# Kernel tuning notes

Hardware: AMD Instinct MI355X
Metric: run time of the kernel (lower is better)

## Reference

```python
import jax, jax.numpy as jnp
import numpy as np

EPS = 1e-5


def setup_inputs() -> dict:
    key = jax.random.key(0)
    ks = jax.random.split(key, 4)
    N, E, D, L = 100000, 1600000, 128, 3
    x = jax.random.normal(ks[0], (N, D), dtype=jnp.float32)
    edge_index = jax.random.randint(ks[1], (2, E), 0, N, dtype=jnp.int64)
    # torch Linear weight layout [out, in]; kaiming-ish scale
    W = jax.random.normal(ks[2], (L, D, D), dtype=jnp.float32) / np.sqrt(D)
    b = jnp.zeros((L, D), dtype=jnp.float32)
    gamma = jnp.ones((L, D), dtype=jnp.float32)
    beta = jnp.zeros((L, D), dtype=jnp.float32)
    return {"x": x, "edge_index": edge_index, "W": W, "b": b,
            "gamma": gamma, "beta": beta}


def reference(x, edge_index, W, b, gamma, beta):
    N = x.shape[0]
    L = W.shape[0]
    # add_self_loops
    loops = jnp.arange(N, dtype=edge_index.dtype)
    ei = jnp.concatenate([edge_index, jnp.stack([loops, loops])], axis=1)
    row, col = ei[0], ei[1]  # source, target (PyG source_to_target flow)
    # degree of target nodes (includes self loops)
    deg = jax.ops.segment_sum(jnp.ones(col.shape, x.dtype), col, num_segments=N)
    deg_inv_sqrt = jnp.where(deg > 0, deg ** -0.5, jnp.array(0.0, x.dtype))
    norm = deg_inv_sqrt[row] * deg_inv_sqrt[col]  # [E+N]
    for l in range(L):
        h = x @ W[l].T  # Linear, no bias
        # gather source messages, scale, scatter-add to targets
        out = jax.ops.segment_sum(norm[:, None] * h[row], col, num_segments=N)
        out = out + b[l]
        # NodeNorm 'm': subtract per-node (row) mean over features
        out = out - jnp.mean(out, axis=1, keepdims=True)
        # BatchNorm1d (training mode: biased batch stats over node axis)
        mu = jnp.mean(out, axis=0)
        var = jnp.var(out, axis=0)
        x = gamma[l] * (out - mu) * jax.lax.rsqrt(var + EPS) + beta[l]
    return x
```

## Files before the change

### kernel.cpp

```cpp
#include <hip/hip_runtime.h>

#define D 128
#define EPSV 1e-5f

typedef _Float16 f16;
typedef __attribute__((ext_vector_type(8))) _Float16 f16x8;
typedef __attribute__((ext_vector_type(4))) _Float16 f16x4;
typedef __attribute__((ext_vector_type(4))) float f32x4;

__global__ __launch_bounds__(256) void cvt_kernel(const float* __restrict__ x,
                                                  f16* __restrict__ xh, long long total4) {
    long long i = (long long)blockIdx.x * blockDim.x + threadIdx.x;
    const long long stride = (long long)gridDim.x * blockDim.x;
    for (; i < total4; i += stride) {
        float4 v = reinterpret_cast<const float4*>(x)[i];
        f16x4 o;
        o[0] = (f16)v.x; o[1] = (f16)v.y; o[2] = (f16)v.z; o[3] = (f16)v.w;
        reinterpret_cast<f16x4*>(xh)[i] = o;
    }
}

__global__ void fold_kernel(const float* __restrict__ W, const float* __restrict__ scsh,
                            int use_id, f16* __restrict__ Wfo, float* __restrict__ shW) {
    const int o = blockIdx.x;
    const int k = threadIdx.x;
    float w = W[o * D + k];
    float sc = use_id ? 1.0f : scsh[k];
    float sh = use_id ? 0.0f : scsh[D + k];
    Wfo[o * D + k] = (f16)(w * sc);
    float v = sh * w;
    #pragma unroll
    for (int off = 1; off < 64; off <<= 1) v += __shfl_xor(v, off, 64);
    __shared__ float red[2];
    if ((k & 63) == 0) red[k >> 6] = v;
    __syncthreads();
    if (k == 0) shW[o] = red[0] + red[1];
}


__global__ __launch_bounds__(256) void bcount_kernel(const int* __restrict__ col,
                                                     int* __restrict__ gb, int E, int seg) {
    __shared__ int s[4096];
    for (int j = threadIdx.x; j < seg; j += 256) s[j] = 0;
    __syncthreads();
    int i = blockIdx.x * 256 + threadIdx.x;
    const int stride = gridDim.x * 256;
    for (; i < E; i += stride) {
        int b = col[i] >> 8;
        int p = (i >> 8) & 7;
        atomicAdd(&s[b * 8 + p], 1);
    }
    __syncthreads();
    for (int j = threadIdx.x; j < seg; j += 256)
        if (s[j]) atomicAdd(&gb[j], s[j]);
}

__global__ __launch_bounds__(1024) void bscan_kernel(const int* __restrict__ gb,
                                                     int* __restrict__ soff,
                                                     int* __restrict__ cur) {
    __shared__ int s[1024];
    const int tid = threadIdx.x;
    const int base = tid * 4;
    int g0 = gb[base], g1 = gb[base + 1], g2 = gb[base + 2], g3 = gb[base + 3];
    int my = g0 + g1 + g2 + g3;
    s[tid] = my;
    __syncthreads();
    for (int off = 1; off < 1024; off <<= 1) {
        int t = (tid >= off) ? s[tid - off] : 0;
        __syncthreads();
        s[tid] += t;
        __syncthreads();
    }
    int ex = s[tid] - my;
    soff[base] = ex;           cur[(base + 0) * 16] = ex;  ex += g0;
    soff[base + 1] = ex;       cur[(base + 1) * 16] = ex;  ex += g1;
    soff[base + 2] = ex;       cur[(base + 2) * 16] = ex;  ex += g2;
    soff[base + 3] = ex;       cur[(base + 3) * 16] = ex;
    if (tid == 1023) soff[4096] = s[1023];
}

__global__ __launch_bounds__(256) void bfill_kernel(const int* __restrict__ row,
                                                    const int* __restrict__ col,
                                                    int* __restrict__ cur,
                                                    int2* __restrict__ bpairs, int E) {
    const int p = blockIdx.x & 7;
    int i = blockIdx.x * 256 + threadIdx.x;
    const int stride = gridDim.x * 256;
    for (; i < E; i += stride) {
        int c = col[i];
        int b = c >> 8;
        int pos = atomicAdd(&cur[(b * 8 + p) * 16], 1);
        bpairs[pos] = make_int2(row[i], c);
    }
}

__global__ __launch_bounds__(256) void bdeg_kernel(const int2* __restrict__ bpairs,
                                                   const int* __restrict__ soff,
                                                   int* __restrict__ deg,
                                                   float* __restrict__ dis, int N) {
    __shared__ int dc[256];
    const int b = blockIdx.x;
    const int tid = threadIdx.x;
    dc[tid] = 0;
    __syncthreads();
    const int s0 = soff[b * 8], s1 = soff[(b + 1) * 8];
    for (int k = s0 + tid; k < s1; k += 256)
        atomicAdd(&dc[bpairs[k].y & 255], 1);
    __syncthreads();
    int c = (b << 8) + tid;
    if (c < N) {
        int dv = dc[tid];
        deg[c] = dv;
        dis[c] = rsqrtf((float)dv + 1.0f);
    }
}

__global__ void scan1_kernel(const int* __restrict__ cnt, int* __restrict__ offs,
                             int* __restrict__ bsum, int N) {
    __shared__ int s[256];
    int tid = threadIdx.x;
    int i = blockIdx.x * 256 + tid;
    int v = (i < N) ? cnt[i] : 0;
    s[tid] = v;
    __syncthreads();
    for (int off = 1; off < 256; off <<= 1) {
        int t = (tid >= off) ? s[tid - off] : 0;
        __syncthreads();
        s[tid] += t;
        __syncthreads();
    }
    if (i < N) offs[i] = s[tid] - v;
    if (tid == 255) bsum[blockIdx.x] = s[255];
}

__global__ void scan2_kernel(int* __restrict__ bsum, int NB) {
    __shared__ int s[512];
    int tid = threadIdx.x;
    int v = (tid < NB) ? bsum[tid] : 0;
    s[tid] = v;
    __syncthreads();
    for (int off = 1; off < 512; off <<= 1) {
        int t = (tid >= off) ? s[tid - off] : 0;
        __syncthreads();
        s[tid] += t;
        __syncthreads();
    }
    if (tid < NB) bsum[tid] = s[tid] - v;
}

__global__ void scan3_kernel(int* __restrict__ offs, const int* __restrict__ bsum,
                             int N, int E) {
    int i = blockIdx.x * 256 + threadIdx.x;
    if (i < N) offs[i] += bsum[blockIdx.x];
    if (i == 0) offs[N] = E;
}

__global__ __launch_bounds__(256) void cfill_kernel(const int2* __restrict__ bpairs,
                                                    const int* __restrict__ soff,
                                                    const int* __restrict__ offs,
                                                    int* __restrict__ srcs, int N) {
    __shared__ int lc[256];
    const int b = blockIdx.x;
    const int tid = threadIdx.x;
    int c = (b << 8) + tid;
    lc[tid] = (c < N) ? offs[c] : 0;
    __syncthreads();
    const int s0 = soff[b * 8], s1 = soff[(b + 1) * 8];
    for (int k = s0 + tid; k < s1; k += 256) {
        int2 pr = bpairs[k];
        int pos = atomicAdd(&lc[pr.y & 255], 1);
        srcs[pos] = pr.x;
    }
}


__global__ __launch_bounds__(256) void gemm_kernel(
    const f16* __restrict__ xh, const f16* __restrict__ Wfo,
    const float* __restrict__ shW, const float* __restrict__ dis,
    f16* __restrict__ h, int N, int nrg)
{
    const int lane = threadIdx.x & 63;
    const int l15 = lane & 15;
    const int lh = lane >> 4;

    f16x8 af[8][4];
    #pragma unroll
    for (int t = 0; t < 8; t++)
        #pragma unroll
        for (int kb = 0; kb < 4; kb++)
            af[t][kb] = *reinterpret_cast<const f16x8*>(
                &Wfo[(t * 16 + l15) * D + kb * 32 + lh * 8]);

    const int wid = (blockIdx.x * blockDim.x + threadIdx.x) >> 6;
    const int nwaves = (gridDim.x * blockDim.x) >> 6;

    for (int rg = wid; rg < nrg; rg += nwaves) {
        int row = rg * 16 + l15;
        int rrow = min(row, N - 1);
        f16x8 bf[4];
        #pragma unroll
        for (int kb = 0; kb < 4; kb++)
            bf[kb] = *reinterpret_cast<const f16x8*>(
                &xh[(long long)rrow * D + kb * 32 + lh * 8]);
        float d = dis[rrow];
        bool ok = (row < N);

        #pragma unroll
        for (int t = 0; t < 8; t++) {
            f32x4 acc = {0.0f, 0.0f, 0.0f, 0.0f};
            #pragma unroll
            for (int kb = 0; kb < 4; kb++)
                acc = __builtin_amdgcn_mfma_f32_16x16x32_f16(af[t][kb], bf[kb], acc, 0, 0, 0);
            int o0 = t * 16 + lh * 4;
            float4 sw = *reinterpret_cast<const float4*>(&shW[o0]);
            f16x4 ov;
            ov[0] = (f16)(d * (acc[0] + sw.x));
            ov[1] = (f16)(d * (acc[1] + sw.y));
            ov[2] = (f16)(d * (acc[2] + sw.z));
            ov[3] = (f16)(d * (acc[3] + sw.w));
            if (ok)
                *reinterpret_cast<f16x4*>(&h[(long long)row * D + o0]) = ov;
        }
    }
}

__global__ __launch_bounds__(256) void gather_kernel(
    const f16* __restrict__ h, const int* __restrict__ offs,
    const int* __restrict__ srcs, const float* __restrict__ dis,
    const float* __restrict__ bias, f16* __restrict__ t,
    float* __restrict__ stats, int N)
{
    const int tid = threadIdx.x;
    const int l16 = tid & 15;
    const int grp = tid >> 4;
    const int f8 = l16 * 8;
    float bv[8];
    {
        float4 ba = *reinterpret_cast<const float4*>(&bias[f8]);
        float4 bb = *reinterpret_cast<const float4*>(&bias[f8 + 4]);
        bv[0] = ba.x; bv[1] = ba.y; bv[2] = ba.z; bv[3] = ba.w;
        bv[4] = bb.x; bv[5] = bb.y; bv[6] = bb.z; bv[7] = bb.w;
    }
    float ssum[8] = {0, 0, 0, 0, 0, 0, 0, 0}, ssq[8] = {0, 0, 0, 0, 0, 0, 0, 0};

    for (int c = blockIdx.x * 16 + grp; c < N; c += gridDim.x * 16) {
        f16x8 hv = *reinterpret_cast<const f16x8*>(&h[(long long)c * D + f8]);
        float a[8], a2[8];
        #pragma unroll
        for (int m = 0; m < 8; m++) { a[m] = (float)hv[m]; a2[m] = 0.0f; }
        const int k0 = offs[c], k1 = offs[c + 1];
        for (int kb = k0; kb < k1; kb += 16) {
            int kk = kb + l16;
            int rl = (kk < k1) ? srcs[kk] : 0;
            int cnt = min(16, k1 - kb);
            int j = 0;
            for (; j + 2 <= cnt; j += 2) {
                int r0 = __shfl(rl, j, 16);
                int r1 = __shfl(rl, j + 1, 16);
                f16x8 v0 = *reinterpret_cast<const f16x8*>(&h[(long long)r0 * D + f8]);
                f16x8 v1 = *reinterpret_cast<const f16x8*>(&h[(long long)r1 * D + f8]);
                #pragma unroll
                for (int m = 0; m < 8; m++) { a[m] += (float)v0[m]; a2[m] += (float)v1[m]; }
            }
            if (j < cnt) {
                int r0 = __shfl(rl, j, 16);
                f16x8 v0 = *reinterpret_cast<const f16x8*>(&h[(long long)r0 * D + f8]);
                #pragma unroll
                for (int m = 0; m < 8; m++) a[m] += (float)v0[m];
            }
        }
        float d = dis[c];
        float tv[8];
        float s = 0.0f;
        #pragma unroll
        for (int m = 0; m < 8; m++) {
            tv[m] = d * (a[m] + a2[m]) + bv[m];
            s += tv[m];
        }
        #pragma unroll
        for (int off = 1; off < 16; off <<= 1) s += __shfl_xor(s, off, 16);
        float mean = s * (1.0f / 128.0f);
        f16x8 ov;
        #pragma unroll
        for (int m = 0; m < 8; m++) {
            tv[m] -= mean;
            ov[m] = (f16)tv[m];
            ssum[m] += tv[m];
            ssq[m] += tv[m] * tv[m];
        }
        *reinterpret_cast<f16x8*>(&t[(long long)c * D + f8]) = ov;
    }

    __shared__ float red[256 * 16];
    #pragma unroll
    for (int j = 0; j < 8; j++) {
        red[tid * 16 + j] = ssum[j];
        red[tid * 16 + 8 + j] = ssq[j];
    }
    __syncthreads();
    const int o = tid;
    const int f = o & 127;
    const int sq = o >> 7;
    const int lf = f >> 3;
    const int j = f & 7;
    float v = 0;
    #pragma unroll
    for (int g = 0; g < 16; g++)
        v += red[(g * 16 + lf) * 16 + sq * 8 + j];
    unsafeAtomicAdd(&stats[o], v);
}

__global__ void stats_kernel(const float* __restrict__ stats,
                             const float* __restrict__ gamma,
                             const float* __restrict__ beta,
                             float* __restrict__ scsh, float Ninv)
{
    int j = threadIdx.x;
    float mu = stats[j] * Ninv;
    float var = stats[D + j] * Ninv - mu * mu;
    float inv = rsqrtf(var + EPSV);
    float sc = gamma[j] * inv;
    scsh[j] = sc;
    scsh[D + j] = beta[j] - mu * sc;
}

__global__ __launch_bounds__(256) void epi2_kernel(
    const f16* __restrict__ t, const float* __restrict__ scsh,
    float* __restrict__ out, long long total4)
{
    __shared__ float sc[D], sh[D];
    if (threadIdx.x < D) {
        sc[threadIdx.x] = scsh[threadIdx.x];
        sh[threadIdx.x] = scsh[D + threadIdx.x];
    }
    __syncthreads();
    long long i = (long long)blockIdx.x * blockDim.x + threadIdx.x;
    const long long stride = (long long)gridDim.x * blockDim.x;
    for (; i < total4; i += stride) {
        f16x4 v = reinterpret_cast<const f16x4*>(t)[i];
        int f0 = (int)((i * 4) & (D - 1));
        float4 o;
        o.x = (float)v[0] * sc[f0 + 0] + sh[f0 + 0];
        o.y = (float)v[1] * sc[f0 + 1] + sh[f0 + 1];
        o.z = (float)v[2] * sc[f0 + 2] + sh[f0 + 2];
        o.w = (float)v[3] * sc[f0 + 3] + sh[f0 + 3];
        reinterpret_cast<float4*>(out)[i] = o;
    }
}

extern "C" void kernel_launch(void* const* d_in, const int* in_sizes, int n_in,
                              void* d_out, int out_size, void* d_ws, size_t ws_size,
                              hipStream_t stream)
{
    const float* x_in  = (const float*)d_in[0];
    const int*   ei    = (const int*)d_in[1];
    const float* W     = (const float*)d_in[2];
    const float* bias  = (const float*)d_in[3];
    const float* gamma = (const float*)d_in[4];
    const float* beta  = (const float*)d_in[5];

    const int N = in_sizes[0] / D;
    const int E = in_sizes[1] / 2;
    const int L = in_sizes[2] / (D * D);
    const int* row = ei;
    const int* col = ei + E;
    const int NB = (N + 255) / 256;
    const int NBUCK = (N + 255) >> 8;
    const int seg = NBUCK * 8;
    const int nrg = (N + 15) / 16;

    f16* tbuf = (f16*)d_ws;
    f16* hbuf = tbuf + (size_t)N * D;
    f16* Wfo  = hbuf + (size_t)N * D;
    float* dis   = (float*)(Wfo + D * D);
    float* stats = dis + N;
    float* scsh  = stats + 2 * D;
    float* shW   = scsh + 2 * D;
    int* deg  = (int*)(shW + D);
    int* offs = deg + N;
    int* srcs = offs + (N + 1);
    int* bsum = srcs + E;
    int* gb   = bsum + 512;
    int* soff = gb + 4096;
    int* cur  = soff + 4097;
    size_t cur_end = (size_t)(cur + 4096 * 16 - (int*)d_ws);
    int2* bpairs = (int2*)((int*)d_ws + ((cur_end + 1) & ~(size_t)1));

    hipMemsetAsync(gb, 0, 4096 * sizeof(int), stream);
    bcount_kernel<<<128, 256, 0, stream>>>(col, gb, E, seg);
    bscan_kernel<<<1, 1024, 0, stream>>>(gb, soff, cur);
    bfill_kernel<<<1024, 256, 0, stream>>>(row, col, cur, bpairs, E);
    bdeg_kernel<<<NBUCK, 256, 0, stream>>>(bpairs, soff, deg, dis, N);
    scan1_kernel<<<NB, 256, 0, stream>>>(deg, offs, bsum, N);
    scan2_kernel<<<1, 512, 0, stream>>>(bsum, NB);
    scan3_kernel<<<NB, 256, 0, stream>>>(offs, bsum, N, E);
    cfill_kernel<<<NBUCK, 256, 0, stream>>>(bpairs, soff, offs, srcs, N);

    const float Ninv = 1.0f / (float)N;
    const long long total4 = (long long)N * D / 4;

    cvt_kernel<<<2048, 256, 0, stream>>>(x_in, tbuf, total4);
    fold_kernel<<<D, D, 0, stream>>>(W, scsh, 1, Wfo, shW);

    for (int l = 0; l < L; l++) {
        gemm_kernel<<<512, 256, 0, stream>>>(tbuf, Wfo, shW, dis, hbuf, N, nrg);
        hipMemsetAsync(stats, 0, 2 * D * sizeof(float), stream);
        gather_kernel<<<2048, 256, 0, stream>>>(
            hbuf, offs, srcs, dis, bias + (size_t)l * D, tbuf, stats, N);
        stats_kernel<<<1, D, 0, stream>>>(
            stats, gamma + (size_t)l * D, beta + (size_t)l * D, scsh, Ninv);
        if (l < L - 1)
            fold_kernel<<<D, D, 0, stream>>>(W + (size_t)(l + 1) * D * D, scsh, 0, Wfo, shW);
        else
            epi2_kernel<<<4096, 256, 0, stream>>>(tbuf, scsh, (float*)d_out, total4);
    }
}
```

Measured before the change: 527.6 us.

## Order gather nodes by degree, fuse input conversion into GEMM, unroll gather

Adds a counting-sort pass that orders target nodes by descending in-degree, and the gather kernel walks nodes in that order so that 16-lane groups in a wave get similar edge counts. The separate fp32-to-fp16 conversion kernel is removed, and the first-layer GEMM reads fp32 input directly and converts in registers. The gather inner loop is unrolled to four loads per step, and bfill now picks its partition from the edge index rather than the block index. Costs are three small setup kernels, an extra indirection per node in the gather, and the loss of contiguous node access for the output and self rows.

```diff
diff --git a/kernel.cpp b/kernel.cpp
--- a/kernel.cpp
+++ b/kernel.cpp
@@ -7,18 +7,6 @@
 typedef __attribute__((ext_vector_type(8))) _Float16 f16x8;
 typedef __attribute__((ext_vector_type(4))) _Float16 f16x4;
 typedef __attribute__((ext_vector_type(4))) float f32x4;
-
-__global__ __launch_bounds__(256) void cvt_kernel(const float* __restrict__ x,
-                                                  f16* __restrict__ xh, long long total4) {
-    long long i = (long long)blockIdx.x * blockDim.x + threadIdx.x;
-    const long long stride = (long long)gridDim.x * blockDim.x;
-    for (; i < total4; i += stride) {
-        float4 v = reinterpret_cast<const float4*>(x)[i];
-        f16x4 o;
-        o[0] = (f16)v.x; o[1] = (f16)v.y; o[2] = (f16)v.z; o[3] = (f16)v.w;
-        reinterpret_cast<f16x4*>(xh)[i] = o;
-    }
-}
 
 __global__ void fold_kernel(const float* __restrict__ W, const float* __restrict__ scsh,
                             int use_id, f16* __restrict__ Wfo, float* __restrict__ shW) {
@@ -37,7 +25,6 @@
     if (k == 0) shW[o] = red[0] + red[1];
 }
 
-
 __global__ __launch_bounds__(256) void bcount_kernel(const int* __restrict__ col,
                                                      int* __restrict__ gb, int E, int seg) {
     __shared__ int s[4096];
@@ -83,12 +70,12 @@
                                                     const int* __restrict__ col,
                                                     int* __restrict__ cur,
                                                     int2* __restrict__ bpairs, int E) {
-    const int p = blockIdx.x & 7;
     int i = blockIdx.x * 256 + threadIdx.x;
     const int stride = gridDim.x * 256;
     for (; i < E; i += stride) {
         int c = col[i];
         int b = c >> 8;
+        int p = (i >> 8) & 7;
         int pos = atomicAdd(&cur[(b * 8 + p) * 16], 1);
         bpairs[pos] = make_int2(row[i], c);
     }
@@ -173,11 +160,51 @@
     }
 }
 
+__global__ __launch_bounds__(256) void dhist_kernel(const int* __restrict__ deg,
+                                                    int* __restrict__ hist, int N) {
+    __shared__ int s[256];
+    s[threadIdx.x] = 0;
+    __syncthreads();
+    int i = blockIdx.x * 256 + threadIdx.x;
+    const int stride = gridDim.x * 256;
+    for (; i < N; i += stride)
+        atomicAdd(&s[255 - min(deg[i], 255)], 1);
+    __syncthreads();
+    if (s[threadIdx.x]) atomicAdd(&hist[threadIdx.x], s[threadIdx.x]);
+}
+
+__global__ void dscan_kernel(const int* __restrict__ hist, int* __restrict__ bcur) {
+    __shared__ int s[256];
+    int tid = threadIdx.x;
+    int v = hist[tid];
+    s[tid] = v;
+    __syncthreads();
+    for (int off = 1; off < 256; off <<= 1) {
+        int t = (tid >= off) ? s[tid - off] : 0;
+        __syncthreads();
+        s[tid] += t;
+        __syncthreads();
+    }
+    bcur[tid * 16] = s[tid] - v;
+}
+
+__global__ __launch_bounds__(256) void dorder_kernel(const int* __restrict__ deg,
+                                                     int* __restrict__ bcur,
+                                                     int* __restrict__ order, int N) {
+    int i = blockIdx.x * 256 + threadIdx.x;
+    const int stride = gridDim.x * 256;
+    for (; i < N; i += stride) {
+        int b = 255 - min(deg[i], 255);
+        int pos = atomicAdd(&bcur[b * 16], 1);
+        order[pos] = i;
+    }
+}
+
 
 __global__ __launch_bounds__(256) void gemm_kernel(
-    const f16* __restrict__ xh, const f16* __restrict__ Wfo,
-    const float* __restrict__ shW, const float* __restrict__ dis,
-    f16* __restrict__ h, int N, int nrg)
+    const f16* __restrict__ xh, const float* __restrict__ xf32,
+    const f16* __restrict__ Wfo, const float* __restrict__ shW,
+    const float* __restrict__ dis, f16* __restrict__ h, int N, int nrg)
 {
     const int lane = threadIdx.x & 63;
     const int l15 = lane & 15;
@@ -198,10 +225,23 @@
         int row = rg * 16 + l15;
         int rrow = min(row, N - 1);
         f16x8 bf[4];
-        #pragma unroll
-        for (int kb = 0; kb < 4; kb++)
-            bf[kb] = *reinterpret_cast<const f16x8*>(
-                &xh[(long long)rrow * D + kb * 32 + lh * 8]);
+        if (xf32) {
+            #pragma unroll
+            for (int kb = 0; kb < 4; kb++) {
+                const float* p = &xf32[(long long)rrow * D + kb * 32 + lh * 8];
+                float4 u0 = *reinterpret_cast<const float4*>(p);
+                float4 u1 = *reinterpret_cast<const float4*>(p + 4);
+                f16x8 b;
+                b[0] = (f16)u0.x; b[1] = (f16)u0.y; b[2] = (f16)u0.z; b[3] = (f16)u0.w;
+                b[4] = (f16)u1.x; b[5] = (f16)u1.y; b[6] = (f16)u1.z; b[7] = (f16)u1.w;
+                bf[kb] = b;
+            }
+        } else {
+            #pragma unroll
+            for (int kb = 0; kb < 4; kb++)
+                bf[kb] = *reinterpret_cast<const f16x8*>(
+                    &xh[(long long)rrow * D + kb * 32 + lh * 8]);
+        }
         float d = dis[rrow];
         bool ok = (row < N);
 
@@ -226,9 +266,9 @@
 
 __global__ __launch_bounds__(256) void gather_kernel(
     const f16* __restrict__ h, const int* __restrict__ offs,
-    const int* __restrict__ srcs, const float* __restrict__ dis,
-    const float* __restrict__ bias, f16* __restrict__ t,
-    float* __restrict__ stats, int N)
+    const int* __restrict__ srcs, const int* __restrict__ order,
+    const float* __restrict__ dis, const float* __restrict__ bias,
+    f16* __restrict__ t, float* __restrict__ stats, int N)
 {
     const int tid = threadIdx.x;
     const int l16 = tid & 15;
@@ -243,7 +283,8 @@
     }
     float ssum[8] = {0, 0, 0, 0, 0, 0, 0, 0}, ssq[8] = {0, 0, 0, 0, 0, 0, 0, 0};
 
-    for (int c = blockIdx.x * 16 + grp; c < N; c += gridDim.x * 16) {
+    for (int ci = blockIdx.x * 16 + grp; ci < N; ci += gridDim.x * 16) {
+        const int c = order[ci];
         f16x8 hv = *reinterpret_cast<const f16x8*>(&h[(long long)c * D + f8]);
         float a[8], a2[8];
         #pragma unroll
@@ -254,15 +295,22 @@
             int rl = (kk < k1) ? srcs[kk] : 0;
             int cnt = min(16, k1 - kb);
             int j = 0;
-            for (; j + 2 <= cnt; j += 2) {
+            for (; j + 4 <= cnt; j += 4) {
                 int r0 = __shfl(rl, j, 16);
                 int r1 = __shfl(rl, j + 1, 16);
+                int r2 = __shfl(rl, j + 2, 16);
+                int r3 = __shfl(rl, j + 3, 16);
                 f16x8 v0 = *reinterpret_cast<const f16x8*>(&h[(long long)r0 * D + f8]);
                 f16x8 v1 = *reinterpret_cast<const f16x8*>(&h[(long long)r1 * D + f8]);
+                f16x8 v2 = *reinterpret_cast<const f16x8*>(&h[(long long)r2 * D + f8]);
+                f16x8 v3 = *reinterpret_cast<const f16x8*>(&h[(long long)r3 * D + f8]);
                 #pragma unroll
-                for (int m = 0; m < 8; m++) { a[m] += (float)v0[m]; a2[m] += (float)v1[m]; }
+                for (int m = 0; m < 8; m++) {
+                    a[m] += (float)v0[m] + (float)v2[m];
+                    a2[m] += (float)v1[m] + (float)v3[m];
+                }
             }
-            if (j < cnt) {
+            for (; j < cnt; j++) {
                 int r0 = __shfl(rl, j, 16);
                 f16x8 v0 = *reinterpret_cast<const f16x8*>(&h[(long long)r0 * D + f8]);
                 #pragma unroll
@@ -376,17 +424,21 @@
     float* stats = dis + N;
     float* scsh  = stats + 2 * D;
     float* shW   = scsh + 2 * D;
-    int* deg  = (int*)(shW + D);
-    int* offs = deg + N;
-    int* srcs = offs + (N + 1);
-    int* bsum = srcs + E;
-    int* gb   = bsum + 512;
-    int* soff = gb + 4096;
-    int* cur  = soff + 4097;
-    size_t cur_end = (size_t)(cur + 4096 * 16 - (int*)d_ws);
-    int2* bpairs = (int2*)((int*)d_ws + ((cur_end + 1) & ~(size_t)1));
+    int* deg   = (int*)(shW + D);
+    int* offs  = deg + N;
+    int* srcs  = offs + (N + 1);
+    int* bsum  = srcs + E;
+    int* gb    = bsum + 512;
+    int* soff  = gb + 4096;
+    int* cur   = soff + 4097;
+    int* hist  = cur + 4096 * 16;
+    int* bcur  = hist + 256;
+    int* order = bcur + 256 * 16;
+    size_t used = (size_t)(order + N - (int*)d_ws);
+    int2* bpairs = (int2*)((int*)d_ws + ((used + 1) & ~(size_t)1));
 
     hipMemsetAsync(gb, 0, 4096 * sizeof(int), stream);
+    hipMemsetAsync(hist, 0, 256 * sizeof(int), stream);
     bcount_kernel<<<128, 256, 0, stream>>>(col, gb, E, seg);
     bscan_kernel<<<1, 1024, 0, stream>>>(gb, soff, cur);
     bfill_kernel<<<1024, 256, 0, stream>>>(row, col, cur, bpairs, E);
@@ -395,18 +447,21 @@
     scan2_kernel<<<1, 512, 0, stream>>>(bsum, NB);
     scan3_kernel<<<NB, 256, 0, stream>>>(offs, bsum, N, E);
     cfill_kernel<<<NBUCK, 256, 0, stream>>>(bpairs, soff, offs, srcs, N);
+    dhist_kernel<<<128, 256, 0, stream>>>(deg, hist, N);
+    dscan_kernel<<<1, 256, 0, stream>>>(hist, bcur);
+    dorder_kernel<<<128, 256, 0, stream>>>(deg, bcur, order, N);
 
     const float Ninv = 1.0f / (float)N;
     const long long total4 = (long long)N * D / 4;
 
-    cvt_kernel<<<2048, 256, 0, stream>>>(x_in, tbuf, total4);
     fold_kernel<<<D, D, 0, stream>>>(W, scsh, 1, Wfo, shW);
 
     for (int l = 0; l < L; l++) {
-        gemm_kernel<<<512, 256, 0, stream>>>(tbuf, Wfo, shW, dis, hbuf, N, nrg);
+        gemm_kernel<<<512, 256, 0, stream>>>(
+            tbuf, (l == 0) ? x_in : nullptr, Wfo, shW, dis, hbuf, N, nrg);
         hipMemsetAsync(stats, 0, 2 * D * sizeof(float), stream);
         gather_kernel<<<2048, 256, 0, stream>>>(
-            hbuf, offs, srcs, dis, bias + (size_t)l * D, tbuf, stats, N);
+            hbuf, offs, srcs, order, dis, bias + (size_t)l * D, tbuf, stats, N);
         stats_kernel<<<1, D, 0, stream>>>(
             stats, gamma + (size_t)l * D, beta + (size_t)l * D, scsh, Ninv);
         if (l < L - 1)
```

Measured after the change: 705.9 us. +33.8%, slower.
